# Kernel tuning notes

Hardware: AMD Instinct MI355X
Metric: run time of the kernel (lower is better)

The kernel has to match this reference:

```python
import jax, jax.numpy as jnp
import numpy as np

HIDDEN = 128
HEADS = 8
HEAD_DIM = HIDDEN // HEADS
N = 2048
SCALE = HEAD_DIM ** -0.5


def setup_inputs() -> dict:
    key = jax.random.key(0)
    ks = jax.random.split(key, 12)
    # xavier_uniform bound for square (HIDDEN, HIDDEN) weights
    bound = float(np.sqrt(6.0 / (HIDDEN + HIDDEN)))
    def w(k):
        return jax.random.uniform(k, (HIDDEN, HIDDEN), jnp.float32, -bound, bound)
    return {
        "x": jax.random.normal(ks[0], (N, HIDDEN), jnp.float32),
        "attention_bias": jax.random.normal(ks[1], (N, N, HEADS), jnp.float32),
        "key_padding_mask": jnp.zeros((N,), jnp.bool_),
        "Wq": w(ks[2]), "bq": jnp.zeros((HIDDEN,), jnp.float32),
        "Wk": w(ks[3]), "bk": jnp.zeros((HIDDEN,), jnp.float32),
        "Wv": w(ks[4]), "bv": jnp.zeros((HIDDEN,), jnp.float32),
        "Wo": w(ks[5]), "bo": jnp.zeros((HIDDEN,), jnp.float32),
    }


def reference(x, attention_bias, key_padding_mask, Wq, bq, Wk, bk, Wv, bv, Wo, bo):
    n = x.shape[0]
    # torch Linear: y = x @ W.T + b
    q = (x @ Wq.T + bq).reshape(n, HEADS, HEAD_DIM).transpose(1, 0, 2)  # (H, N, D)
    k = (x @ Wk.T + bk).reshape(n, HEADS, HEAD_DIM).transpose(1, 0, 2)
    v = (x @ Wv.T + bv).reshape(n, HEADS, HEAD_DIM).transpose(1, 0, 2)
    scores = jnp.einsum('hnd,hmd->hnm', q, k) * SCALE        # (H, N, N)
    scores = scores + attention_bias.transpose(2, 0, 1)       # additive graph bias
    mask = key_padding_mask[None, None, :]                    # (1, 1, N) over keys
    scores = jnp.where(mask, -jnp.inf, scores)
    attn = jax.nn.softmax(scores, axis=-1)
    out = jnp.einsum('hnm,hmd->hnd', attn, v)                 # (H, N, D)
    out = out.transpose(1, 0, 2).reshape(n, HIDDEN)
    return out @ Wo.T + bo
```

## Files before the change

### kernel.cpp

```cpp
#include <hip/hip_runtime.h>
#include <hip/hip_bf16.h>

#define NSEQ 2048
#define HID 128
#define HEADS 8
#define HD 16
#define SCALE 0.25f
#define TQ 16
#define SPLIT 8
#define KEYS_PER (NSEQ / SPLIT)
#define KT16 (KEYS_PER / 16)
#define NS 132

typedef unsigned short ushort_t;
typedef __attribute__((ext_vector_type(4))) short short4v;
typedef __attribute__((ext_vector_type(4))) float floatx4;
typedef __attribute__((ext_vector_type(4))) float f32x4;

__device__ __forceinline__ unsigned pack_bf16x2(float a, float b) {
    __hip_bfloat16 ba = __float2bfloat16(a);
    __hip_bfloat16 bb = __float2bfloat16(b);
    return (unsigned)*(ushort_t*)&ba | ((unsigned)*(ushort_t*)&bb << 16);
}

__global__ __launch_bounds__(128) void qkv_kernel(
    const float* __restrict__ x, const float* __restrict__ Wq,
    const float* __restrict__ Wk, const float* __restrict__ Wv,
    const float* __restrict__ bq, const float* __restrict__ bk,
    const float* __restrict__ bv,
    __hip_bfloat16* __restrict__ Qh, __hip_bfloat16* __restrict__ Ql,
    __hip_bfloat16* __restrict__ Kb, __hip_bfloat16* __restrict__ Vt)
{
    __shared__ float xs[8 * HID];
    const int j = threadIdx.x;
    const int mat = blockIdx.x >> 8;
    const int rb = blockIdx.x & 255;
    const int r0 = rb * 8;
    const float* W = (mat == 0) ? Wq : (mat == 1) ? Wk : Wv;
    const float* bb = (mat == 0) ? bq : (mat == 1) ? bk : bv;
    const float4* xg = (const float4*)(x + (size_t)r0 * HID);
    float4* xl = (float4*)xs;
    for (int i = j; i < 8 * HID / 4; i += 128) xl[i] = xg[i];
    __syncthreads();
    float acc[8];
#pragma unroll
    for (int r = 0; r < 8; ++r) acc[r] = 0.f;
    const float4* Wrow = (const float4*)(W + (size_t)j * HID);
#pragma unroll 4
    for (int i4 = 0; i4 < HID / 4; ++i4) {
        float4 wv = Wrow[i4];
#pragma unroll
        for (int r = 0; r < 8; ++r) {
            float4 xv = *(const float4*)&xs[r * HID + i4 * 4];
            acc[r] = fmaf(xv.x, wv.x, acc[r]);
            acc[r] = fmaf(xv.y, wv.y, acc[r]);
            acc[r] = fmaf(xv.z, wv.z, acc[r]);
            acc[r] = fmaf(xv.w, wv.w, acc[r]);
        }
    }
    float bv_ = bb[j];
#pragma unroll
    for (int r = 0; r < 8; ++r) acc[r] += bv_;
    if (mat == 0) {
#pragma unroll
        for (int r = 0; r < 8; ++r) {
            float qsv = acc[r] * SCALE;
            __hip_bfloat16 hb = __float2bfloat16(qsv);
            float hf = __bfloat162float(hb);
            __hip_bfloat16 lb = __float2bfloat16(qsv - hf);
            Qh[(size_t)(r0 + r) * HID + j] = hb;
            Ql[(size_t)(r0 + r) * HID + j] = lb;
        }
    } else if (mat == 1) {
#pragma unroll
        for (int r = 0; r < 8; ++r) Kb[(size_t)(r0 + r) * HID + j] = __float2bfloat16(acc[r]);
    } else {
        unsigned u[4];
#pragma unroll
        for (int p = 0; p < 4; ++p) u[p] = pack_bf16x2(acc[2 * p], acc[2 * p + 1]);
        *(uint4*)((ushort_t*)Vt + (size_t)j * NSEQ + r0) = make_uint4(u[0], u[1], u[2], u[3]);
    }
}

__global__ __launch_bounds__(256, 6) void attn_kernel(
    const __hip_bfloat16* __restrict__ Qh, const __hip_bfloat16* __restrict__ Ql,
    const __hip_bfloat16* __restrict__ Kb, const __hip_bfloat16* __restrict__ Vt,
    const float* __restrict__ bias, const unsigned char* __restrict__ mask,
    float* __restrict__ Op, float* __restrict__ Lp)
{
    __shared__ float bs[2][16 * NS];

    const int t = threadIdx.x;
    const int lane = t & 63;
    const int wid = t >> 6;
    const int qi = lane & 15;
    const int g = lane >> 4;
    const int qb = blockIdx.x & 127;
    const int sp = blockIdx.x >> 7;
    const int n0 = qb * TQ;
    const int m0 = sp * KEYS_PER;
    const int h0 = wid * 2;

    const int sn = t >> 4;
    const int sc = t & 15;
    const float* brow = bias + (size_t)(n0 + sn) * (NSEQ * HEADS) + (size_t)(m0 + sc) * HEADS;
    const int wbase = sn * NS + sc;

    short4v qhf[2], qlf[2];
#pragma unroll
    for (int hh = 0; hh < 2; ++hh) {
        const size_t qoff = (size_t)(n0 + qi) * HID + (h0 + hh) * HD + 4 * g;
        qhf[hh] = *(const short4v*)((const ushort_t*)Qh + qoff);
        qlf[hh] = *(const short4v*)((const ushort_t*)Ql + qoff);
    }

    floatx4 o[2];
    o[0] = (floatx4){0.f, 0.f, 0.f, 0.f};
    o[1] = (floatx4){0.f, 0.f, 0.f, 0.f};
    float lrun[2] = {0.f, 0.f};

    f32x4 st0 = __builtin_nontemporal_load((const f32x4*)brow);
    f32x4 st1 = __builtin_nontemporal_load((const f32x4*)(brow + 4));

#pragma unroll 2
    for (int kt = 0; kt < KT16; ++kt) {
        float* B = &bs[kt & 1][0];
        B[wbase]       = st0.x; B[wbase + 16]  = st0.y;
        B[wbase + 32]  = st0.z; B[wbase + 48]  = st0.w;
        B[wbase + 64]  = st1.x; B[wbase + 80]  = st1.y;
        B[wbase + 96]  = st1.z; B[wbase + 112] = st1.w;
        __syncthreads();
        if (kt + 1 < KT16) {
            const float* bnext = brow + (size_t)(kt + 1) * 16 * HEADS;
            st0 = __builtin_nontemporal_load((const f32x4*)bnext);
            st1 = __builtin_nontemporal_load((const f32x4*)(bnext + 4));
        }
        const int m1 = m0 + kt * 16;
        const uchar4 mk = *(const uchar4*)(mask + m1 + 4 * g);
#pragma unroll
        for (int hh = 0; hh < 2; ++hh) {
            const int h = h0 + hh;
            short4v ka = *(const short4v*)((const ushort_t*)Kb +
                         (size_t)(m1 + qi) * HID + h * HD + 4 * g);
            floatx4 s = *(const f32x4*)&B[qi * NS + h * 16 + 4 * g];
            s = __builtin_amdgcn_mfma_f32_16x16x16bf16_1k(ka, qhf[hh], s, 0, 0, 0);
            s = __builtin_amdgcn_mfma_f32_16x16x16bf16_1k(ka, qlf[hh], s, 0, 0, 0);
            float e0 = mk.x ? 0.f : __expf(s.x);
            float e1 = mk.y ? 0.f : __expf(s.y);
            float e2 = mk.z ? 0.f : __expf(s.z);
            float e3 = mk.w ? 0.f : __expf(s.w);
            lrun[hh] += (e0 + e1) + (e2 + e3);
            __hip_bfloat16 p0 = __float2bfloat16(e0);
            __hip_bfloat16 p1 = __float2bfloat16(e1);
            __hip_bfloat16 p2 = __float2bfloat16(e2);
            __hip_bfloat16 p3 = __float2bfloat16(e3);
            short4v pa = {(short)*(ushort_t*)&p0, (short)*(ushort_t*)&p1,
                          (short)*(ushort_t*)&p2, (short)*(ushort_t*)&p3};
            short4v vb = *(const short4v*)((const ushort_t*)Vt +
                         (size_t)(h * HD + qi) * NSEQ + m1 + 4 * g);
            o[hh] = __builtin_amdgcn_mfma_f32_16x16x16bf16_1k(pa, vb, o[hh], 0, 0, 0);
        }
    }

#pragma unroll
    for (int hh = 0; hh < 2; ++hh) {
        lrun[hh] += __shfl_xor(lrun[hh], 16);
        lrun[hh] += __shfl_xor(lrun[hh], 32);
        const int h = h0 + hh;
#pragma unroll
        for (int r = 0; r < 4; ++r)
            Op[((size_t)(n0 + 4 * g + r) * SPLIT + sp) * HID + h * HD + qi] = o[hh][r];
        if (g == 0)
            Lp[((size_t)(n0 + qi) * SPLIT + sp) * HEADS + h] = lrun[hh];
    }
}

__global__ __launch_bounds__(128) void proj_kernel(
    const float* __restrict__ Op, const float* __restrict__ Lp,
    const float* __restrict__ Wo, const float* __restrict__ bo,
    float* __restrict__ out)
{
    __shared__ float xs[4 * HID];
    const int j = threadIdx.x;
    const int r0 = blockIdx.x * 4;
    const int hh = j >> 4;
#pragma unroll
    for (int r = 0; r < 4; ++r) {
        const size_t n = r0 + r;
        float s = 0.f, l = 0.f;
#pragma unroll
        for (int sp = 0; sp < SPLIT; ++sp) {
            s += Op[(n * SPLIT + sp) * HID + j];
            l += Lp[(n * SPLIT + sp) * HEADS + hh];
        }
        xs[r * HID + j] = s / l;
    }
    __syncthreads();
    float acc[4];
#pragma unroll
    for (int r = 0; r < 4; ++r) acc[r] = 0.f;
    const float4* Wrow = (const float4*)(Wo + (size_t)j * HID);
#pragma unroll 4
    for (int i4 = 0; i4 < HID / 4; ++i4) {
        float4 wv = Wrow[i4];
#pragma unroll
        for (int r = 0; r < 4; ++r) {
            float4 xv = *(const float4*)&xs[r * HID + i4 * 4];
            acc[r] = fmaf(xv.x, wv.x, acc[r]);
            acc[r] = fmaf(xv.y, wv.y, acc[r]);
            acc[r] = fmaf(xv.z, wv.z, acc[r]);
            acc[r] = fmaf(xv.w, wv.w, acc[r]);
        }
    }
    float b = bo[j];
#pragma unroll
    for (int r = 0; r < 4; ++r)
        out[(size_t)(r0 + r) * HID + j] = acc[r] + b;
}

extern "C" void kernel_launch(void* const* d_in, const int* in_sizes, int n_in,
                              void* d_out, int out_size, void* d_ws, size_t ws_size,
                              hipStream_t stream) {
    const float* x    = (const float*)d_in[0];
    const float* bias = (const float*)d_in[1];
    const unsigned char* mask = (const unsigned char*)d_in[2];
    const float* Wq = (const float*)d_in[3];
    const float* bq = (const float*)d_in[4];
    const float* Wk = (const float*)d_in[5];
    const float* bk = (const float*)d_in[6];
    const float* Wv = (const float*)d_in[7];
    const float* bv = (const float*)d_in[8];
    const float* Wo = (const float*)d_in[9];
    const float* bo = (const float*)d_in[10];
    float* out = (float*)d_out;

    float* w = (float*)d_ws;
    __hip_bfloat16* Qh = (__hip_bfloat16*)(w);
    __hip_bfloat16* Ql = (__hip_bfloat16*)(w + 131072);
    __hip_bfloat16* Kb = (__hip_bfloat16*)(w + 262144);
    __hip_bfloat16* Vt = (__hip_bfloat16*)(w + 393216);
    float* Op  = w + 524288;
    float* Lp  = w + 524288 + (size_t)NSEQ * SPLIT * HID;

    qkv_kernel<<<768, 128, 0, stream>>>(x, Wq, Wk, Wv, bq, bk, bv, Qh, Ql, Kb, Vt);
    attn_kernel<<<128 * SPLIT, 256, 0, stream>>>(Qh, Ql, Kb, Vt, bias, mask, Op, Lp);
    proj_kernel<<<512, 128, 0, stream>>>(Op, Lp, Wo, bo, out);
}
```

Measured before the change: 255.7 us.

## Give each wave all heads for its own query tile with per-wave bias buffers

The attention kernel is restructured so each wave owns a 16-query tile and handles all 8 heads, not 2 heads of a shared tile. Each wave stages its own bias slice into a private double-buffered LDS region, which removes the block-wide __syncthreads. The grid shrinks from 1024 to 256 blocks and each wave keeps 8 accumulators plus Q fragments in registers. This cuts barrier cost and reuses each K/V fragment across more work, but it raises register pressure and leaves far fewer waves to hide the latency of the bias stream.

```diff
diff --git a/kernel.cpp b/kernel.cpp
--- a/kernel.cpp
+++ b/kernel.cpp
@@ -6,11 +6,10 @@
 #define HEADS 8
 #define HD 16
 #define SCALE 0.25f
-#define TQ 16
 #define SPLIT 8
 #define KEYS_PER (NSEQ / SPLIT)
-#define KT16 (KEYS_PER / 16)
-#define NS 132
+#define KT (KEYS_PER / 16)
+#define S_LDS 132
 
 typedef unsigned short ushort_t;
 typedef __attribute__((ext_vector_type(4))) short short4v;
@@ -82,74 +81,86 @@
     }
 }
 
-__global__ __launch_bounds__(256, 6) void attn_kernel(
+__global__ __launch_bounds__(256, 2) void attn_kernel(
     const __hip_bfloat16* __restrict__ Qh, const __hip_bfloat16* __restrict__ Ql,
     const __hip_bfloat16* __restrict__ Kb, const __hip_bfloat16* __restrict__ Vt,
     const float* __restrict__ bias, const unsigned char* __restrict__ mask,
     float* __restrict__ Op, float* __restrict__ Lp)
 {
-    __shared__ float bs[2][16 * NS];
+    __shared__ float bs[4][2][16 * S_LDS];
 
     const int t = threadIdx.x;
     const int lane = t & 63;
     const int wid = t >> 6;
     const int qi = lane & 15;
     const int g = lane >> 4;
-    const int qb = blockIdx.x & 127;
-    const int sp = blockIdx.x >> 7;
-    const int n0 = qb * TQ;
+    const int sq = lane >> 2;
+    const int mc = lane & 3;
+    const int h4 = (mc & 1) * 4;
+    const int par = mc >> 1;
+
+    const int nb = blockIdx.x & 31;
+    const int sp = blockIdx.x >> 5;
+    const int n0 = nb * 64 + wid * 16;
     const int m0 = sp * KEYS_PER;
-    const int h0 = wid * 2;
-
-    const int sn = t >> 4;
-    const int sc = t & 15;
-    const float* brow = bias + (size_t)(n0 + sn) * (NSEQ * HEADS) + (size_t)(m0 + sc) * HEADS;
-    const int wbase = sn * NS + sc;
-
-    short4v qhf[2], qlf[2];
-#pragma unroll
-    for (int hh = 0; hh < 2; ++hh) {
-        const size_t qoff = (size_t)(n0 + qi) * HID + (h0 + hh) * HD + 4 * g;
-        qhf[hh] = *(const short4v*)((const ushort_t*)Qh + qoff);
-        qlf[hh] = *(const short4v*)((const ushort_t*)Ql + qoff);
-    }
-
-    floatx4 o[2];
-    o[0] = (floatx4){0.f, 0.f, 0.f, 0.f};
-    o[1] = (floatx4){0.f, 0.f, 0.f, 0.f};
-    float lrun[2] = {0.f, 0.f};
-
-    f32x4 st0 = __builtin_nontemporal_load((const f32x4*)brow);
-    f32x4 st1 = __builtin_nontemporal_load((const f32x4*)(brow + 4));
+
+    short4v qhf[8], qlf[8];
+#pragma unroll
+    for (int h = 0; h < 8; ++h) {
+        const size_t qoff = (size_t)(n0 + qi) * HID + h * HD + 4 * g;
+        qhf[h] = *(const short4v*)((const ushort_t*)Qh + qoff);
+        qlf[h] = *(const short4v*)((const ushort_t*)Ql + qoff);
+    }
+
+    floatx4 o[8];
+    float lrun[8];
+#pragma unroll
+    for (int h = 0; h < 8; ++h) {
+        o[h] = (floatx4){0.f, 0.f, 0.f, 0.f};
+        lrun[h] = 0.f;
+    }
+
+    const float* bbase = bias + (size_t)(n0 + sq) * (NSEQ * HEADS)
+                              + (size_t)m0 * HEADS + mc * 4;
+
+    {
+        f32x4 nx[8];
+#pragma unroll
+        for (int p = 0; p < 8; ++p)
+            nx[p] = __builtin_nontemporal_load((const f32x4*)(bbase + p * 16));
+        float* B0 = &bs[wid][0][0];
+#pragma unroll
+        for (int p = 0; p < 8; ++p)
+#pragma unroll
+            for (int jj = 0; jj < 4; ++jj)
+                B0[sq * S_LDS + (h4 + jj) * 16 + 2 * p + par] = nx[p][jj];
+    }
 
 #pragma unroll 2
-    for (int kt = 0; kt < KT16; ++kt) {
-        float* B = &bs[kt & 1][0];
-        B[wbase]       = st0.x; B[wbase + 16]  = st0.y;
-        B[wbase + 32]  = st0.z; B[wbase + 48]  = st0.w;
-        B[wbase + 64]  = st1.x; B[wbase + 80]  = st1.y;
-        B[wbase + 96]  = st1.z; B[wbase + 112] = st1.w;
-        __syncthreads();
-        if (kt + 1 < KT16) {
-            const float* bnext = brow + (size_t)(kt + 1) * 16 * HEADS;
-            st0 = __builtin_nontemporal_load((const f32x4*)bnext);
-            st1 = __builtin_nontemporal_load((const f32x4*)(bnext + 4));
-        }
+    for (int kt = 0; kt < KT; ++kt) {
+        float* B  = &bs[wid][kt & 1][0];
+        float* Bn = &bs[wid][(kt + 1) & 1][0];
         const int m1 = m0 + kt * 16;
+        f32x4 pf[8];
+        if (kt + 1 < KT) {
+#pragma unroll
+            for (int p = 0; p < 8; ++p)
+                pf[p] = __builtin_nontemporal_load(
+                            (const f32x4*)(bbase + (kt + 1) * 128 + p * 16));
+        }
         const uchar4 mk = *(const uchar4*)(mask + m1 + 4 * g);
 #pragma unroll
-        for (int hh = 0; hh < 2; ++hh) {
-            const int h = h0 + hh;
+        for (int h = 0; h < 8; ++h) {
             short4v ka = *(const short4v*)((const ushort_t*)Kb +
                          (size_t)(m1 + qi) * HID + h * HD + 4 * g);
-            floatx4 s = *(const f32x4*)&B[qi * NS + h * 16 + 4 * g];
-            s = __builtin_amdgcn_mfma_f32_16x16x16bf16_1k(ka, qhf[hh], s, 0, 0, 0);
-            s = __builtin_amdgcn_mfma_f32_16x16x16bf16_1k(ka, qlf[hh], s, 0, 0, 0);
+            floatx4 s = *(const f32x4*)&B[qi * S_LDS + h * 16 + 4 * g];
+            s = __builtin_amdgcn_mfma_f32_16x16x16bf16_1k(ka, qhf[h], s, 0, 0, 0);
+            s = __builtin_amdgcn_mfma_f32_16x16x16bf16_1k(ka, qlf[h], s, 0, 0, 0);
             float e0 = mk.x ? 0.f : __expf(s.x);
             float e1 = mk.y ? 0.f : __expf(s.y);
             float e2 = mk.z ? 0.f : __expf(s.z);
             float e3 = mk.w ? 0.f : __expf(s.w);
-            lrun[hh] += (e0 + e1) + (e2 + e3);
+            lrun[h] += (e0 + e1) + (e2 + e3);
             __hip_bfloat16 p0 = __float2bfloat16(e0);
             __hip_bfloat16 p1 = __float2bfloat16(e1);
             __hip_bfloat16 p2 = __float2bfloat16(e2);
@@ -158,20 +169,26 @@
                           (short)*(ushort_t*)&p2, (short)*(ushort_t*)&p3};
             short4v vb = *(const short4v*)((const ushort_t*)Vt +
                          (size_t)(h * HD + qi) * NSEQ + m1 + 4 * g);
-            o[hh] = __builtin_amdgcn_mfma_f32_16x16x16bf16_1k(pa, vb, o[hh], 0, 0, 0);
-        }
-    }
-
-#pragma unroll
-    for (int hh = 0; hh < 2; ++hh) {
-        lrun[hh] += __shfl_xor(lrun[hh], 16);
-        lrun[hh] += __shfl_xor(lrun[hh], 32);
-        const int h = h0 + hh;
+            o[h] = __builtin_amdgcn_mfma_f32_16x16x16bf16_1k(pa, vb, o[h], 0, 0, 0);
+        }
+        if (kt + 1 < KT) {
+#pragma unroll
+            for (int p = 0; p < 8; ++p)
+#pragma unroll
+                for (int jj = 0; jj < 4; ++jj)
+                    Bn[sq * S_LDS + (h4 + jj) * 16 + 2 * p + par] = pf[p][jj];
+        }
+    }
+
+#pragma unroll
+    for (int h = 0; h < 8; ++h) {
+        lrun[h] += __shfl_xor(lrun[h], 16);
+        lrun[h] += __shfl_xor(lrun[h], 32);
 #pragma unroll
         for (int r = 0; r < 4; ++r)
-            Op[((size_t)(n0 + 4 * g + r) * SPLIT + sp) * HID + h * HD + qi] = o[hh][r];
+            Op[((size_t)(n0 + 4 * g + r) * SPLIT + sp) * HID + h * HD + qi] = o[h][r];
         if (g == 0)
-            Lp[((size_t)(n0 + qi) * SPLIT + sp) * HEADS + h] = lrun[hh];
+            Lp[((size_t)(n0 + qi) * SPLIT + sp) * HEADS + h] = lrun[h];
     }
 }
 
@@ -243,6 +260,6 @@
     float* Lp  = w + 524288 + (size_t)NSEQ * SPLIT * HID;
 
     qkv_kernel<<<768, 128, 0, stream>>>(x, Wq, Wk, Wv, bq, bk, bv, Qh, Ql, Kb, Vt);
-    attn_kernel<<<128 * SPLIT, 256, 0, stream>>>(Qh, Ql, Kb, Vt, bias, mask, Op, Lp);
+    attn_kernel<<<32 * SPLIT, 256, 0, stream>>>(Qh, Ql, Kb, Vt, bias, mask, Op, Lp);
     proj_kernel<<<512, 128, 0, stream>>>(Op, Lp, Wo, bo, out);
 }
```

New measurement: 252.8 us. Within noise of the previous version (-1.1%).

## Load bias directly into registers and split key tiles across wave pairs

Applied to the files above, without the earlier changes.

The attention kernel stops staging the bias through double-buffered shared memory with a per-tile __syncthreads. Each wave now reads its own bias values straight from global memory into registers, handling four heads, with register double-buffering. The two wave pairs take alternating key tiles and combine their partial outputs and row sums through shared memory at the end. This removes the per-tile barriers and LDS traffic, but raises register pressure (occupancy hint lowered to 4) and makes the bias loads narrower and strided.

```diff
diff --git a/kernel.cpp b/kernel.cpp
--- a/kernel.cpp
+++ b/kernel.cpp
@@ -6,11 +6,9 @@
 #define HEADS 8
 #define HD 16
 #define SCALE 0.25f
-#define TQ 16
 #define SPLIT 8
 #define KEYS_PER (NSEQ / SPLIT)
-#define KT16 (KEYS_PER / 16)
-#define NS 132
+#define OWN_T 8
 
 typedef unsigned short ushort_t;
 typedef __attribute__((ext_vector_type(4))) short short4v;
@@ -82,73 +80,75 @@
     }
 }
 
-__global__ __launch_bounds__(256, 6) void attn_kernel(
+__global__ __launch_bounds__(256, 4) void attn_kernel(
     const __hip_bfloat16* __restrict__ Qh, const __hip_bfloat16* __restrict__ Ql,
     const __hip_bfloat16* __restrict__ Kb, const __hip_bfloat16* __restrict__ Vt,
     const float* __restrict__ bias, const unsigned char* __restrict__ mask,
     float* __restrict__ Op, float* __restrict__ Lp)
 {
-    __shared__ float bs[2][16 * NS];
+    __shared__ float ob[2][16][64];
+    __shared__ float lr[2][4][16];
 
     const int t = threadIdx.x;
     const int lane = t & 63;
     const int wid = t >> 6;
     const int qi = lane & 15;
     const int g = lane >> 4;
-    const int qb = blockIdx.x & 127;
+    const int h0 = (wid & 1) * 4;
+    const int par = wid >> 1;
+
+    const int nb = blockIdx.x & 127;
     const int sp = blockIdx.x >> 7;
-    const int n0 = qb * TQ;
+    const int n0 = nb * 16;
     const int m0 = sp * KEYS_PER;
-    const int h0 = wid * 2;
-
-    const int sn = t >> 4;
-    const int sc = t & 15;
-    const float* brow = bias + (size_t)(n0 + sn) * (NSEQ * HEADS) + (size_t)(m0 + sc) * HEADS;
-    const int wbase = sn * NS + sc;
-
-    short4v qhf[2], qlf[2];
-#pragma unroll
-    for (int hh = 0; hh < 2; ++hh) {
+
+    short4v qhf[4], qlf[4];
+#pragma unroll
+    for (int hh = 0; hh < 4; ++hh) {
         const size_t qoff = (size_t)(n0 + qi) * HID + (h0 + hh) * HD + 4 * g;
         qhf[hh] = *(const short4v*)((const ushort_t*)Qh + qoff);
         qlf[hh] = *(const short4v*)((const ushort_t*)Ql + qoff);
     }
 
-    floatx4 o[2];
-    o[0] = (floatx4){0.f, 0.f, 0.f, 0.f};
-    o[1] = (floatx4){0.f, 0.f, 0.f, 0.f};
-    float lrun[2] = {0.f, 0.f};
-
-    f32x4 st0 = __builtin_nontemporal_load((const f32x4*)brow);
-    f32x4 st1 = __builtin_nontemporal_load((const f32x4*)(brow + 4));
-
-#pragma unroll 2
-    for (int kt = 0; kt < KT16; ++kt) {
-        float* B = &bs[kt & 1][0];
-        B[wbase]       = st0.x; B[wbase + 16]  = st0.y;
-        B[wbase + 32]  = st0.z; B[wbase + 48]  = st0.w;
-        B[wbase + 64]  = st1.x; B[wbase + 80]  = st1.y;
-        B[wbase + 96]  = st1.z; B[wbase + 112] = st1.w;
-        __syncthreads();
-        if (kt + 1 < KT16) {
-            const float* bnext = brow + (size_t)(kt + 1) * 16 * HEADS;
-            st0 = __builtin_nontemporal_load((const f32x4*)bnext);
-            st1 = __builtin_nontemporal_load((const f32x4*)(bnext + 4));
-        }
+    floatx4 o[4];
+    float lrun[4];
+#pragma unroll
+    for (int hh = 0; hh < 4; ++hh) {
+        o[hh] = (floatx4){0.f, 0.f, 0.f, 0.f};
+        lrun[hh] = 0.f;
+    }
+
+    const float* bb = bias + ((size_t)(n0 + qi) * NSEQ + m0 + 4 * g) * HEADS + h0;
+
+    f32x4 bufA[4], bufB[4];
+#pragma unroll
+    for (int r = 0; r < 4; ++r)
+        bufA[r] = *(const f32x4*)(bb + par * (16 * HEADS) + r * HEADS);
+
+    auto body = [&](int i, f32x4* cur, f32x4* nxt) {
+        const int kt = 2 * i + par;
         const int m1 = m0 + kt * 16;
+        floatx4 s[4];
+#pragma unroll
+        for (int hh = 0; hh < 4; ++hh)
+            s[hh] = (floatx4){cur[0][hh], cur[1][hh], cur[2][hh], cur[3][hh]};
+        if (i + 1 < OWN_T) {
+            const float* bn = bb + (size_t)(2 * (i + 1) + par) * (16 * HEADS);
+#pragma unroll
+            for (int r = 0; r < 4; ++r) nxt[r] = *(const f32x4*)(bn + r * HEADS);
+        }
         const uchar4 mk = *(const uchar4*)(mask + m1 + 4 * g);
 #pragma unroll
-        for (int hh = 0; hh < 2; ++hh) {
+        for (int hh = 0; hh < 4; ++hh) {
             const int h = h0 + hh;
             short4v ka = *(const short4v*)((const ushort_t*)Kb +
                          (size_t)(m1 + qi) * HID + h * HD + 4 * g);
-            floatx4 s = *(const f32x4*)&B[qi * NS + h * 16 + 4 * g];
-            s = __builtin_amdgcn_mfma_f32_16x16x16bf16_1k(ka, qhf[hh], s, 0, 0, 0);
-            s = __builtin_amdgcn_mfma_f32_16x16x16bf16_1k(ka, qlf[hh], s, 0, 0, 0);
-            float e0 = mk.x ? 0.f : __expf(s.x);
-            float e1 = mk.y ? 0.f : __expf(s.y);
-            float e2 = mk.z ? 0.f : __expf(s.z);
-            float e3 = mk.w ? 0.f : __expf(s.w);
+            floatx4 sv = __builtin_amdgcn_mfma_f32_16x16x16bf16_1k(ka, qhf[hh], s[hh], 0, 0, 0);
+            sv = __builtin_amdgcn_mfma_f32_16x16x16bf16_1k(ka, qlf[hh], sv, 0, 0, 0);
+            float e0 = mk.x ? 0.f : __expf(sv.x);
+            float e1 = mk.y ? 0.f : __expf(sv.y);
+            float e2 = mk.z ? 0.f : __expf(sv.z);
+            float e3 = mk.w ? 0.f : __expf(sv.w);
             lrun[hh] += (e0 + e1) + (e2 + e3);
             __hip_bfloat16 p0 = __float2bfloat16(e0);
             __hip_bfloat16 p1 = __float2bfloat16(e1);
@@ -160,18 +160,42 @@
                          (size_t)(h * HD + qi) * NSEQ + m1 + 4 * g);
             o[hh] = __builtin_amdgcn_mfma_f32_16x16x16bf16_1k(pa, vb, o[hh], 0, 0, 0);
         }
-    }
-
-#pragma unroll
-    for (int hh = 0; hh < 2; ++hh) {
+    };
+
+#pragma unroll
+    for (int i = 0; i < OWN_T; i += 2) {
+        body(i, bufA, bufB);
+        body(i + 1, bufB, bufA);
+    }
+
+#pragma unroll
+    for (int hh = 0; hh < 4; ++hh) {
         lrun[hh] += __shfl_xor(lrun[hh], 16);
         lrun[hh] += __shfl_xor(lrun[hh], 32);
-        const int h = h0 + hh;
-#pragma unroll
-        for (int r = 0; r < 4; ++r)
-            Op[((size_t)(n0 + 4 * g + r) * SPLIT + sp) * HID + h * HD + qi] = o[hh][r];
-        if (g == 0)
-            Lp[((size_t)(n0 + qi) * SPLIT + sp) * HEADS + h] = lrun[hh];
+    }
+    if (par == 1) {
+#pragma unroll
+        for (int hh = 0; hh < 4; ++hh) {
+#pragma unroll
+            for (int r = 0; r < 4; ++r) ob[wid & 1][hh * 4 + r][lane] = o[hh][r];
+            if (g == 0) lr[wid & 1][hh][qi] = lrun[hh];
+        }
+    }
+    __syncthreads();
+    if (par == 0) {
+#pragma unroll
+        for (int hh = 0; hh < 4; ++hh) {
+            const int h = h0 + hh;
+#pragma unroll
+            for (int r = 0; r < 4; ++r) {
+                float v = o[hh][r] + ob[wid & 1][hh * 4 + r][lane];
+                Op[((size_t)(n0 + 4 * g + r) * SPLIT + sp) * HID + h * HD + qi] = v;
+            }
+            if (g == 0) {
+                float l = lrun[hh] + lr[wid & 1][hh][qi];
+                Lp[((size_t)(n0 + qi) * SPLIT + sp) * HEADS + h] = l;
+            }
+        }
     }
 }
 
```

Measured after the change: 257.8 us. About the same (+0.8%).

## Stage K and V tiles through LDS with coalesced bias loads

Applied to the files above, without the earlier changes.

V is now stored row-major instead of transposed. The attention kernel cooperatively loads 16-key K and V tiles into double-buffered shared memory alongside the bias tile, and builds the V MFMA operand from LDS with scalar gathers. Bias loads are reshaped so each thread reads contiguous float4 along the head dimension, and nontemporal hints are dropped. Occupancy hint lowered from 6 to 4 waves to fit the larger LDS. This is meant to replace scattered global K/V fragment loads with coalesced loads, at the cost of more LDS traffic and four 16-bit LDS reads per V fragment.

```diff
diff --git a/kernel.cpp b/kernel.cpp
--- a/kernel.cpp
+++ b/kernel.cpp
@@ -6,22 +6,16 @@
 #define HEADS 8
 #define HD 16
 #define SCALE 0.25f
-#define TQ 16
 #define SPLIT 8
 #define KEYS_PER (NSEQ / SPLIT)
-#define KT16 (KEYS_PER / 16)
-#define NS 132
+#define NT (KEYS_PER / 16)
+#define SB 132
+#define SKV 68
 
 typedef unsigned short ushort_t;
 typedef __attribute__((ext_vector_type(4))) short short4v;
 typedef __attribute__((ext_vector_type(4))) float floatx4;
 typedef __attribute__((ext_vector_type(4))) float f32x4;
-
-__device__ __forceinline__ unsigned pack_bf16x2(float a, float b) {
-    __hip_bfloat16 ba = __float2bfloat16(a);
-    __hip_bfloat16 bb = __float2bfloat16(b);
-    return (unsigned)*(ushort_t*)&ba | ((unsigned)*(ushort_t*)&bb << 16);
-}
 
 __global__ __launch_bounds__(128) void qkv_kernel(
     const float* __restrict__ x, const float* __restrict__ Wq,
@@ -29,7 +23,7 @@
     const float* __restrict__ bq, const float* __restrict__ bk,
     const float* __restrict__ bv,
     __hip_bfloat16* __restrict__ Qh, __hip_bfloat16* __restrict__ Ql,
-    __hip_bfloat16* __restrict__ Kb, __hip_bfloat16* __restrict__ Vt)
+    __hip_bfloat16* __restrict__ Kb, __hip_bfloat16* __restrict__ Vm)
 {
     __shared__ float xs[8 * HID];
     const int j = threadIdx.x;
@@ -75,36 +69,48 @@
 #pragma unroll
         for (int r = 0; r < 8; ++r) Kb[(size_t)(r0 + r) * HID + j] = __float2bfloat16(acc[r]);
     } else {
-        unsigned u[4];
-#pragma unroll
-        for (int p = 0; p < 4; ++p) u[p] = pack_bf16x2(acc[2 * p], acc[2 * p + 1]);
-        *(uint4*)((ushort_t*)Vt + (size_t)j * NSEQ + r0) = make_uint4(u[0], u[1], u[2], u[3]);
-    }
-}
-
-__global__ __launch_bounds__(256, 6) void attn_kernel(
+#pragma unroll
+        for (int r = 0; r < 8; ++r) Vm[(size_t)(r0 + r) * HID + j] = __float2bfloat16(acc[r]);
+    }
+}
+
+__global__ __launch_bounds__(256, 4) void attn_kernel(
     const __hip_bfloat16* __restrict__ Qh, const __hip_bfloat16* __restrict__ Ql,
-    const __hip_bfloat16* __restrict__ Kb, const __hip_bfloat16* __restrict__ Vt,
+    const __hip_bfloat16* __restrict__ Kb, const __hip_bfloat16* __restrict__ Vm,
     const float* __restrict__ bias, const unsigned char* __restrict__ mask,
     float* __restrict__ Op, float* __restrict__ Lp)
 {
-    __shared__ float bs[2][16 * NS];
+    __shared__ float bsh[2][16 * SB];
+    __shared__ float ksh[2][16 * SKV];
+    __shared__ float vsh[2][16 * SKV];
 
     const int t = threadIdx.x;
     const int lane = t & 63;
     const int wid = t >> 6;
     const int qi = lane & 15;
     const int g = lane >> 4;
+    const int h0 = wid * 2;
+
     const int qb = blockIdx.x & 127;
     const int sp = blockIdx.x >> 7;
-    const int n0 = qb * TQ;
+    const int n0 = qb * 16;
     const int m0 = sp * KEYS_PER;
-    const int h0 = wid * 2;
-
-    const int sn = t >> 4;
-    const int sc = t & 15;
-    const float* brow = bias + (size_t)(n0 + sn) * (NSEQ * HEADS) + (size_t)(m0 + sc) * HEADS;
-    const int wbase = sn * NS + sc;
+
+    const int bq = t >> 5;
+    const int bc = t & 31;
+    const int kq = t >> 4;
+    const int kc = t & 15;
+
+    const float* bA = bias + ((size_t)(n0 + bq) * NSEQ + m0) * HEADS + bc * 4;
+    const float* bB = bias + ((size_t)(n0 + 8 + bq) * NSEQ + m0) * HEADS + bc * 4;
+    const ushort_t* kG = (const ushort_t*)Kb + (size_t)(m0 + kq) * HID + kc * 8;
+    const ushort_t* vG = (const ushort_t*)Vm + (size_t)(m0 + kq) * HID + kc * 8;
+
+    const int bm = bc >> 1;
+    const int bh = 4 * (bc & 1);
+    const int wA = bq * SB + bh * 16 + bm;
+    const int wB = (8 + bq) * SB + bh * 16 + bm;
+    const int wK = kq * SKV + kc * 4;
 
     short4v qhf[2], qlf[2];
 #pragma unroll
@@ -119,30 +125,36 @@
     o[1] = (floatx4){0.f, 0.f, 0.f, 0.f};
     float lrun[2] = {0.f, 0.f};
 
-    f32x4 st0 = __builtin_nontemporal_load((const f32x4*)brow);
-    f32x4 st1 = __builtin_nontemporal_load((const f32x4*)(brow + 4));
-
-#pragma unroll 2
-    for (int kt = 0; kt < KT16; ++kt) {
-        float* B = &bs[kt & 1][0];
-        B[wbase]       = st0.x; B[wbase + 16]  = st0.y;
-        B[wbase + 32]  = st0.z; B[wbase + 48]  = st0.w;
-        B[wbase + 64]  = st1.x; B[wbase + 80]  = st1.y;
-        B[wbase + 96]  = st1.z; B[wbase + 112] = st1.w;
+    f32x4 sb0 = *(const f32x4*)bA;
+    f32x4 sb1 = *(const f32x4*)bB;
+    f32x4 sk  = *(const f32x4*)kG;
+    f32x4 sv  = *(const f32x4*)vG;
+
+    for (int kt = 0; kt < NT; ++kt) {
+        float* Bs = &bsh[kt & 1][0];
+        float* Ks = &ksh[kt & 1][0];
+        float* Vs = &vsh[kt & 1][0];
+        Bs[wA]      = sb0.x; Bs[wA + 16] = sb0.y;
+        Bs[wA + 32] = sb0.z; Bs[wA + 48] = sb0.w;
+        Bs[wB]      = sb1.x; Bs[wB + 16] = sb1.y;
+        Bs[wB + 32] = sb1.z; Bs[wB + 48] = sb1.w;
+        *(f32x4*)&Ks[wK] = sk;
+        *(f32x4*)&Vs[wK] = sv;
         __syncthreads();
-        if (kt + 1 < KT16) {
-            const float* bnext = brow + (size_t)(kt + 1) * 16 * HEADS;
-            st0 = __builtin_nontemporal_load((const f32x4*)bnext);
-            st1 = __builtin_nontemporal_load((const f32x4*)(bnext + 4));
+        if (kt + 1 < NT) {
+            sb0 = *(const f32x4*)(bA + (kt + 1) * (16 * HEADS));
+            sb1 = *(const f32x4*)(bB + (kt + 1) * (16 * HEADS));
+            sk  = *(const f32x4*)(kG + (size_t)(kt + 1) * 16 * HID);
+            sv  = *(const f32x4*)(vG + (size_t)(kt + 1) * 16 * HID);
         }
         const int m1 = m0 + kt * 16;
         const uchar4 mk = *(const uchar4*)(mask + m1 + 4 * g);
+        const ushort_t* vw = (const ushort_t*)Vs;
 #pragma unroll
         for (int hh = 0; hh < 2; ++hh) {
             const int h = h0 + hh;
-            short4v ka = *(const short4v*)((const ushort_t*)Kb +
-                         (size_t)(m1 + qi) * HID + h * HD + 4 * g);
-            floatx4 s = *(const f32x4*)&B[qi * NS + h * 16 + 4 * g];
+            floatx4 s = *(const f32x4*)&Bs[qi * SB + h * 16 + 4 * g];
+            short4v ka = *(const short4v*)&Ks[qi * SKV + h * 8 + 2 * g];
             s = __builtin_amdgcn_mfma_f32_16x16x16bf16_1k(ka, qhf[hh], s, 0, 0, 0);
             s = __builtin_amdgcn_mfma_f32_16x16x16bf16_1k(ka, qlf[hh], s, 0, 0, 0);
             float e0 = mk.x ? 0.f : __expf(s.x);
@@ -156,8 +168,11 @@
             __hip_bfloat16 p3 = __float2bfloat16(e3);
             short4v pa = {(short)*(ushort_t*)&p0, (short)*(ushort_t*)&p1,
                           (short)*(ushort_t*)&p2, (short)*(ushort_t*)&p3};
-            short4v vb = *(const short4v*)((const ushort_t*)Vt +
-                         (size_t)(h * HD + qi) * NSEQ + m1 + 4 * g);
+            ushort_t e0v = vw[(4 * g + 0) * (2 * SKV) + h * 16 + qi];
+            ushort_t e1v = vw[(4 * g + 1) * (2 * SKV) + h * 16 + qi];
+            ushort_t e2v = vw[(4 * g + 2) * (2 * SKV) + h * 16 + qi];
+            ushort_t e3v = vw[(4 * g + 3) * (2 * SKV) + h * 16 + qi];
+            short4v vb = {(short)e0v, (short)e1v, (short)e2v, (short)e3v};
             o[hh] = __builtin_amdgcn_mfma_f32_16x16x16bf16_1k(pa, vb, o[hh], 0, 0, 0);
         }
     }
@@ -238,11 +253,11 @@
     __hip_bfloat16* Qh = (__hip_bfloat16*)(w);
     __hip_bfloat16* Ql = (__hip_bfloat16*)(w + 131072);
     __hip_bfloat16* Kb = (__hip_bfloat16*)(w + 262144);
-    __hip_bfloat16* Vt = (__hip_bfloat16*)(w + 393216);
+    __hip_bfloat16* Vm = (__hip_bfloat16*)(w + 393216);
     float* Op  = w + 524288;
     float* Lp  = w + 524288 + (size_t)NSEQ * SPLIT * HID;
 
-    qkv_kernel<<<768, 128, 0, stream>>>(x, Wq, Wk, Wv, bq, bk, bv, Qh, Ql, Kb, Vt);
-    attn_kernel<<<128 * SPLIT, 256, 0, stream>>>(Qh, Ql, Kb, Vt, bias, mask, Op, Lp);
+    qkv_kernel<<<768, 128, 0, stream>>>(x, Wq, Wk, Wv, bq, bk, bv, Qh, Ql, Kb, Vm);
+    attn_kernel<<<128 * SPLIT, 256, 0, stream>>>(Qh, Ql, Kb, Vm, bias, mask, Op, Lp);
     proj_kernel<<<512, 128, 0, stream>>>(Op, Lp, Wo, bo, out);
 }
```

Result: faster. 237.8 us (-7.0%).
